# Optimization experiments

Measured on AMD Instinct MI355X. Metric: run time of the kernel, lower is better.

The kernel has to match this reference:

```python
import jax, jax.numpy as jnp
import numpy as np

COORD_W, WIDTH_W, VALID_W = 5.0, 1.0, 1.0  # module init defaults
COST_COORD_W, COST_WIDTH_W = 5.0, 1.0      # hardcoded in compute_cost_matrix


def _hungarian(cost):
    """Pure-numpy linear_sum_assignment (Jonker-Volgenant style, e-maxx variant).
    cost: [R, C] float. Returns (row_ind, col_ind) matching scipy semantics
    (min(R, C) pairs minimizing total cost)."""
    cost = np.asarray(cost, dtype=np.float64)
    transposed = cost.shape[0] > cost.shape[1]
    C = cost.T if transposed else cost
    n, m = C.shape  # n <= m
    u = np.zeros(n + 1)
    v = np.zeros(m + 1)
    p = np.zeros(m + 1, dtype=np.int64)   # p[j] = 1-indexed row assigned to col j
    way = np.zeros(m + 1, dtype=np.int64)
    for i in range(1, n + 1):
        p[0] = i
        j0 = 0
        minv = np.full(m + 1, np.inf)
        used = np.zeros(m + 1, dtype=bool)
        while True:
            used[j0] = True
            i0 = p[j0]
            jf = np.nonzero(~used[1:])[0] + 1  # free columns (1-indexed)
            cur = C[i0 - 1, jf - 1] - u[i0] - v[jf]
            upd = cur < minv[jf]
            minv[jf] = np.where(upd, cur, minv[jf])
            way[jf[upd]] = j0
            j1 = jf[np.argmin(minv[jf])]
            delta = minv[j1]
            u[p[used]] += delta
            v[used] -= delta
            minv[jf] -= delta
            j0 = j1
            if p[j0] == 0:
                break
        while j0:
            j1 = way[j0]
            p[j0] = p[j1]
            j0 = j1
    col4row = np.zeros(n, dtype=np.int64)
    for j in range(1, m + 1):
        if p[j] > 0:
            col4row[p[j] - 1] = j - 1
    rows = np.arange(n, dtype=np.int64)
    return (col4row, rows) if transposed else (rows, col4row)


def _compute_matching(pred_strokes, targets):
    """Per-batch Hungarian matching on the (detached) cost matrix.
    Returns padded pred idx P [B,S], gt idx G [B,S], match mask M [B,S], num_gt N [B]."""
    ps = np.asarray(pred_strokes)
    tg = np.asarray(targets)
    B, S, _ = ps.shape
    P = np.zeros((B, S), dtype=np.int64)
    G = np.zeros((B, S), dtype=np.int64)
    M = np.zeros((B, S), dtype=np.float32)
    N = np.zeros((B,), dtype=np.float32)
    for b in range(B):
        valid = np.nonzero(tg[b, :, 10] > 0.5)[0]
        ng = len(valid)
        N[b] = ng
        if ng == 0:
            continue
        gt = tg[b, valid, :10]                      # [ng, 10]
        d = np.abs(ps[b, :, None, :] - gt[None])    # [S, ng, 10]
        cost = COST_COORD_W * d[..., :8].sum(-1) + COST_WIDTH_W * d[..., 8:10].sum(-1)
        pi, gi = _hungarian(cost)
        P[b, :ng] = pi
        G[b, :ng] = valid[gi]
        M[b, :ng] = 1.0
    return P, G, M, N


def _loss(pred_strokes, pred_validity, targets, P, G, M, N):
    gt_strokes = targets[..., :10]
    gt_val = targets[..., 10:11]
    mp = jnp.take_along_axis(pred_strokes, P[..., None], axis=1)  # [B,S,10]
    mg = jnp.take_along_axis(gt_strokes, G[..., None], axis=1)    # [B,S,10]
    ad = jnp.abs(mp - mg) * M[..., None]
    ng = jnp.maximum(N, 1.0)
    coord = ad[..., :8].sum(axis=(1, 2)) / (ng * 8.0)             # per-batch L1 mean
    width = ad[..., 8:10].sum(axis=(1, 2)) / (ng * 2.0)
    # BCE with torch-style log clamp at -100
    logp = jnp.clip(jnp.log(pred_validity), -100.0)
    log1p = jnp.clip(jnp.log(1.0 - pred_validity), -100.0)
    bce = (-(gt_val * logp + (1.0 - gt_val) * log1p)).mean(axis=(1, 2))
    loss_b = jnp.where(N > 0, COORD_W * coord + WIDTH_W * width + VALID_W * bce, bce)
    return loss_b.mean()


def setup_inputs() -> dict:
    key = jax.random.key(0)
    k1, k2, k3 = jax.random.split(key, 3)
    B, S = 256, 64
    return {
        "pred_strokes": jax.random.uniform(k1, (B, S, 10), dtype=jnp.float32),
        "pred_validity": jax.random.uniform(k2, (B, S, 1), dtype=jnp.float32),
        "targets": jax.random.uniform(k3, (B, S, 11), dtype=jnp.float32),
    }


def reference(pred_strokes, pred_validity, targets):
    P, G, M, N = _compute_matching(pred_strokes, targets)
    return _loss(pred_strokes, pred_validity, targets,
                 jnp.asarray(P), jnp.asarray(G), jnp.asarray(M), jnp.asarray(N))
```

## Files before the change

kernel.cpp:

```cpp
#include <hip/hip_runtime.h>
#include <math.h>


#define SS 64
#define LDS_FENCE() asm volatile("s_waitcnt lgkmcnt(0)" ::: "memory")

__device__ __forceinline__ int rlane_i(int x, int lane) {
    return __builtin_amdgcn_readlane(x, lane);
}
__device__ __forceinline__ double rlane_d(double x, int lane) {
    return __hiloint2double(rlane_i(__double2hiint(x), lane),
                            rlane_i(__double2loint(x), lane));
}

template<int CTRL>
__device__ __forceinline__ unsigned dpp_shift_ff(unsigned x) {
    return (unsigned)__builtin_amdgcn_update_dpp(
        (int)0xFFFFFFFFu, (int)x, CTRL, 0xF, 0xF, false);
}
__device__ __forceinline__ unsigned wave_min_u32_to63(unsigned x) {
    unsigned y;
    y = dpp_shift_ff<0x111>(x); x = x < y ? x : y;
    y = dpp_shift_ff<0x112>(x); x = x < y ? x : y;
    y = dpp_shift_ff<0x114>(x); x = x < y ? x : y;
    y = dpp_shift_ff<0x118>(x); x = x < y ? x : y;
    y = dpp_shift_ff<0x142>(x); x = x < y ? x : y;
    y = dpp_shift_ff<0x143>(x); x = x < y ? x : y;
    return x;
}

__global__ __launch_bounds__(64) void detr_match_loss_kernel(
    const float* __restrict__ pred_strokes,
    const float* __restrict__ pred_validity,
    const float* __restrict__ targets,
    double* __restrict__ loss_ws)
{
    const int b = blockIdx.x;
    const int t = threadIdx.x;
    const float* ps = pred_strokes  + (size_t)b * SS * 10;
    const float* pv = pred_validity + (size_t)b * SS;
    const float* tg = targets      + (size_t)b * SS * 11;

    __shared__ float  Cs[SS * SS];
    __shared__ float  tgs[SS * 11];
    __shared__ int    vidx[SS];
    __shared__ int    col4row[SS];

#pragma unroll
    for (int k = 0; k < 11; ++k) tgs[k * SS + t] = tg[k * SS + t];
    LDS_FENCE();

    const float gv    = tgs[t * 11 + 10];
    const bool  valid = gv > 0.5f;
    const unsigned long long vmask = __ballot(valid);
    const int ng = __popcll(vmask);
    if (valid) {
        const int rank = __popcll(vmask & ((1ull << t) - 1ull));
        vidx[rank] = t;
    }
    LDS_FENCE();

    double bterm;
    {
        const float pvv = pv[t];
        const float lp  = fmaxf(logf(pvv), -100.0f);
        const float l1p = fmaxf(logf(1.0f - pvv), -100.0f);
        bterm = -((double)gv * (double)lp + (double)(1.0f - gv) * (double)l1p);
    }

    double csum = 0.0, wsum = 0.0;

    if (ng > 0) {
        float pr[10];
#pragma unroll
        for (int k = 0; k < 10; ++k) pr[k] = ps[t * 10 + k];

        for (int i = 0; i < ng; ++i) {
            const float* g = &tgs[vidx[i] * 11];
            float d[10];
#pragma unroll
            for (int k = 0; k < 10; ++k) d[k] = fabsf(pr[k] - g[k]);
            const float cs = ((d[0] + d[1]) + (d[2] + d[3]))
                           + ((d[4] + d[5]) + (d[6] + d[7]));
            const float wd = d[8] + d[9];
            float c;
            {
#pragma clang fp contract(off)
                c = 5.0f * cs + wd;
            }
            Cs[i * SS + t] = c;
        }

        double v_j   = 0.0;
        double u_reg = 0.0;
        int    p_j   = 0;
        float  Chead = Cs[t];

        for (int i = 1; i <= ng; ++i) {
            double minv_j   = __builtin_inf();
            int    way_j    = 0;
            bool   used_j   = false;
            bool   row_used = (t == i - 1);
            double u0       = 0.0;
            int    j0       = 0;
            float  Cval     = Chead;

            for (;;) {
                used_j = used_j || (t + 1 == j0);
                const double cur = ((double)Cval - u0) - v_j;
                if (!used_j && cur < minv_j) { minv_j = cur; way_j = j0; }

                const unsigned key = used_j ? 0x7FF00000u
                                            : (unsigned)__double2hiint(minv_j);
                const unsigned kr    = wave_min_u32_to63(key);
                const unsigned hstar = (unsigned)rlane_i((int)kr, 63);
                unsigned long long bal = __ballot(key == hstar);
                int j1 = __ffsll(bal);
                int i1 = rlane_i(p_j, j1 - 1);

                float C_next = 0.0f;
                if (i1 != 0) C_next = Cs[(i1 - 1) * SS + t];

                if (__popcll(bal) > 1) {
                    const unsigned lo = (key == hstar)
                        ? (unsigned)__double2loint(minv_j) : 0xFFFFFFFFu;
                    const unsigned lr    = wave_min_u32_to63(lo);
                    const unsigned lstar = (unsigned)rlane_i((int)lr, 63);
                    bal = __ballot(key == hstar && lo == lstar);
                    j1  = __ffsll(bal);
                    i1  = rlane_i(p_j, j1 - 1);
                    if (i1 != 0) C_next = Cs[(i1 - 1) * SS + t];
                }

                const double delta  = rlane_d(minv_j, j1 - 1);
                const double u_next = (i1 != 0) ? rlane_d(u_reg, i1 - 1) : 0.0;

                if (row_used) u_reg += delta;
                if (used_j)   v_j   -= delta;
                else          minv_j -= delta;
                row_used = row_used || (t == i1 - 1);

                j0 = j1;
                if (i1 == 0) break;
                u0 = u_next; Cval = C_next;
            }

            Chead = (i < ng) ? Cs[i * SS + t] : 0.0f;

            int jj = j0;
            while (jj != 0) {
                const int jp   = rlane_i(way_j, jj - 1);
                const int pnew = (jp == 0) ? i : rlane_i(p_j, jp - 1);
                if (t == jj - 1) p_j = pnew;
                jj = jp;
            }
        }

        if (p_j > 0) col4row[p_j - 1] = t;
        LDS_FENCE();

        if (t < ng) {
            const float* g  = &tgs[vidx[t] * 11];
            const float* mp = ps + col4row[t] * 10;
#pragma unroll
            for (int k = 0; k < 8; ++k) csum += (double)fabsf(mp[k] - g[k]);
            wsum = (double)fabsf(mp[8] - g[8]) + (double)fabsf(mp[9] - g[9]);
        }
    }

    double s0 = csum, s1 = wsum, s2 = bterm;
#pragma unroll
    for (int off = 1; off < 64; off <<= 1) {
        s0 += __shfl_xor(s0, off, 64);
        s1 += __shfl_xor(s1, off, 64);
        s2 += __shfl_xor(s2, off, 64);
    }
    if (t == 0) {
        const double bce = s2 / 64.0;
        const double loss = (ng > 0)
            ? 5.0 * (s0 / ((double)ng * 8.0)) + (s1 / ((double)ng * 2.0)) + bce
            : bce;
        loss_ws[b] = loss;
    }
}

__global__ __launch_bounds__(256) void detr_reduce_kernel(
    const double* __restrict__ ws, float* __restrict__ out, int B)
{
    const int t = threadIdx.x;
    double x = 0.0;
    for (int idx = t; idx < B; idx += 256) x += ws[idx];
    for (int off = 1; off < 64; off <<= 1) x += __shfl_xor(x, off, 64);
    __shared__ double part[4];
    if ((t & 63) == 0) part[t >> 6] = x;
    __syncthreads();
    if (t == 0) {
        double s = part[0] + part[1] + part[2] + part[3];
        out[0] = (float)(s / (double)B);
    }
}

extern "C" void kernel_launch(void* const* d_in, const int* in_sizes, int n_in,
                              void* d_out, int out_size, void* d_ws, size_t ws_size,
                              hipStream_t stream) {
    const float* ps = (const float*)d_in[0];
    const float* pv = (const float*)d_in[1];
    const float* tg = (const float*)d_in[2];
    float* out = (float*)d_out;
    double* ws = (double*)d_ws;
    const int B = in_sizes[0] / (SS * 10);

    detr_match_loss_kernel<<<B, SS, 0, stream>>>(ps, pv, tg, ws);
    detr_reduce_kernel<<<1, 256, 0, stream>>>(ws, out, B);
}
```

Baseline: 86.14 us.

## Warm-start Hungarian with greedy row-minimum assignment, augment only free rows

Each row's dual is initialised to its minimum cost, and that minimum column is greedily assigned when it is not yet claimed. The augmenting-path search then runs only for the rows left unassigned. Because the starting duals can make minv negative, the wave-min key is changed to a sign-aware ordering of the double's bits. This is meant to cut the number of Dijkstra iterations per batch. It adds a wave reduction per cost row and may pick a different assignment among equal-cost ties than the reference does.

```diff
diff --git a/kernel.cpp b/kernel.cpp
--- a/kernel.cpp
+++ b/kernel.cpp
@@ -75,6 +75,11 @@
 #pragma unroll
         for (int k = 0; k < 10; ++k) pr[k] = ps[t * 10 + k];
 
+        double u_reg = 0.0;
+        int    p_j   = 0;
+        unsigned long long colclaim = 0ull;
+        unsigned long long freerows = 0ull;
+
         for (int i = 0; i < ng; ++i) {
             const float* g = &tgs[vidx[i] * 11];
             float d[10];
@@ -89,29 +94,45 @@
                 c = 5.0f * cs + wd;
             }
             Cs[i * SS + t] = c;
+
+            const unsigned key = __float_as_uint(c);
+            const unsigned kr  = wave_min_u32_to63(key);
+            const unsigned mst = (unsigned)rlane_i((int)kr, 63);
+            const unsigned long long rbal = __ballot(key == mst);
+            const int jstar = __ffsll(rbal) - 1;
+            if (t == i) u_reg = (double)__uint_as_float(mst);
+            if (!((colclaim >> jstar) & 1ull)) {
+                colclaim |= 1ull << jstar;
+                if (t == jstar) p_j = i + 1;
+            } else {
+                freerows |= 1ull << i;
+            }
         }
 
-        double v_j   = 0.0;
-        double u_reg = 0.0;
-        int    p_j   = 0;
-        float  Chead = Cs[t];
-
-        for (int i = 1; i <= ng; ++i) {
+        double v_j = 0.0;
+
+        while (freerows) {
+            const int r0 = __ffsll(freerows) - 1;
+            freerows &= freerows - 1;
+            const int i = r0 + 1;
+
             double minv_j   = __builtin_inf();
             int    way_j    = 0;
             bool   used_j   = false;
-            bool   row_used = (t == i - 1);
-            double u0       = 0.0;
+            bool   row_used = (t == r0);
+            double u0       = rlane_d(u_reg, r0);
             int    j0       = 0;
-            float  Cval     = Chead;
+            float  Cval     = Cs[r0 * SS + t];
 
             for (;;) {
                 used_j = used_j || (t + 1 == j0);
                 const double cur = ((double)Cval - u0) - v_j;
                 if (!used_j && cur < minv_j) { minv_j = cur; way_j = j0; }
 
-                const unsigned key = used_j ? 0x7FF00000u
-                                            : (unsigned)__double2hiint(minv_j);
+                const unsigned hraw = (unsigned)__double2hiint(minv_j);
+                const bool     mneg = (hraw & 0x80000000u) != 0;
+                const unsigned key  = used_j ? 0xFFFFFFFFu
+                                    : (mneg ? ~hraw : (hraw | 0x80000000u));
                 const unsigned kr    = wave_min_u32_to63(key);
                 const unsigned hstar = (unsigned)rlane_i((int)kr, 63);
                 unsigned long long bal = __ballot(key == hstar);
@@ -122,8 +143,9 @@
                 if (i1 != 0) C_next = Cs[(i1 - 1) * SS + t];
 
                 if (__popcll(bal) > 1) {
-                    const unsigned lo = (key == hstar)
-                        ? (unsigned)__double2loint(minv_j) : 0xFFFFFFFFu;
+                    const unsigned lraw = (unsigned)__double2loint(minv_j);
+                    const unsigned lo   = (key == hstar)
+                                        ? (mneg ? ~lraw : lraw) : 0xFFFFFFFFu;
                     const unsigned lr    = wave_min_u32_to63(lo);
                     const unsigned lstar = (unsigned)rlane_i((int)lr, 63);
                     bal = __ballot(key == hstar && lo == lstar);
@@ -144,8 +166,6 @@
                 if (i1 == 0) break;
                 u0 = u_next; Cval = C_next;
             }
-
-            Chead = (i < ng) ? Cs[i * SS + t] : 0.0f;
 
             int jj = j0;
             while (jj != 0) {
```

After: 84.55 us. Within noise of the previous version (-1.8%).
